# Kernel optimization log

Measured on AMD Instinct MI355X. Metric: run time of the kernel, lower is better.

Reference implementation:

```python
import jax, jax.numpy as jnp
import numpy as np

B_, S_, D_ = 2, 1024, 1024
EXPAND = 2
D_INNER = EXPAND * D_            # 2048
HEADDIM = 64
NHEADS = D_INNER // HEADDIM      # 32
D_STATE = 64
NGROUPS = 1
D_CONV = 4
CONV_DIM = D_INNER + 2 * NGROUPS * D_STATE      # 2176
D_IN_PROJ = 2 * D_INNER + 2 * NGROUPS * D_STATE + NHEADS  # 4256
H_MLP = 8 * D_                   # GatedMLP fc_1 out (scale * d_model)


def setup_inputs() -> dict:
    key = jax.random.key(0)
    ks = jax.random.split(key, 12)
    n = lambda k, shp, s=0.02: jax.random.normal(k, shp, dtype=jnp.float32) * s
    return {
        "x": jax.random.normal(ks[0], (B_, S_, D_), dtype=jnp.float32),
        "in_proj_w": n(ks[1], (D_IN_PROJ, D_)),
        "conv_w": n(ks[2], (CONV_DIM, D_CONV), 0.2),
        "conv_b": jnp.zeros((CONV_DIM,), jnp.float32),
        "dt_bias": jax.random.normal(ks[3], (NHEADS,), dtype=jnp.float32) * 0.5 - 2.0,
        "A_log": jnp.log(1.0 + 15.0 * jax.random.uniform(ks[4], (NHEADS,), dtype=jnp.float32)),
        "D": jax.random.normal(ks[5], (NHEADS,), dtype=jnp.float32) * 0.1 + 1.0,
        "ssm_norm_w": jnp.ones((D_INNER,), jnp.float32),
        "out_proj_w": n(ks[6], (D_, D_INNER)),
        "rms_w": jnp.ones((D_,), jnp.float32),
        "fc1_w": n(ks[7], (H_MLP, D_)),
        "fc2_w": n(ks[8], (D_, H_MLP // 2)),
    }


def _rms(x, w, eps=1e-5):
    return x * jax.lax.rsqrt(jnp.mean(x * x, axis=-1, keepdims=True) + eps) * w


def _mamba(x, in_proj_w, conv_w, conv_b, dt_bias, A_log, D, ssm_norm_w, out_proj_w):
    b, s, _ = x.shape
    zxbcdt = x @ in_proj_w.T                         # [b,s,D_IN_PROJ]
    z = zxbcdt[..., :D_INNER]
    xBC = zxbcdt[..., D_INNER:D_INNER + CONV_DIM]
    dt_raw = zxbcdt[..., -NHEADS:]
    # causal depthwise conv1d + SiLU
    xc = jnp.pad(jnp.transpose(xBC, (0, 2, 1)), ((0, 0), (0, 0), (D_CONV - 1, 0)))
    xc = jax.lax.conv_general_dilated(xc, conv_w[:, None, :], (1,), 'VALID',
                                      feature_group_count=CONV_DIM,
                                      dimension_numbers=('NCH', 'OIH', 'NCH'))
    xBC = jax.nn.silu(jnp.transpose(xc, (0, 2, 1)) + conv_b)
    xs = xBC[..., :D_INNER].reshape(b, s, NHEADS, HEADDIM)
    Bm = xBC[..., D_INNER:D_INNER + D_STATE]         # [b,s,n] (ngroups=1)
    Cm = xBC[..., D_INNER + D_STATE:]
    dt = jax.nn.softplus(dt_raw + dt_bias)           # [b,s,h]
    dA = jnp.exp(dt * (-jnp.exp(A_log)))             # [b,s,h]
    dtx = dt[..., None] * xs                          # [b,s,h,p]

    def step(h, inp):
        dA_t, dtx_t, B_t, C_t = inp
        h = h * dA_t[:, :, None, None] + jnp.einsum('bhp,bn->bhpn', dtx_t, B_t)
        y = jnp.einsum('bhpn,bn->bhp', h, C_t)
        return h, y

    h0 = jnp.zeros((b, NHEADS, HEADDIM, D_STATE), x.dtype)
    _, y = jax.lax.scan(step, h0, (jnp.transpose(dA, (1, 0, 2)),
                                   jnp.transpose(dtx, (1, 0, 2, 3)),
                                   jnp.transpose(Bm, (1, 0, 2)),
                                   jnp.transpose(Cm, (1, 0, 2))))
    y = jnp.transpose(y, (1, 0, 2, 3)) + D[None, None, :, None] * xs
    y = y.reshape(b, s, D_INNER) * jax.nn.silu(z)    # gated
    y = _rms(y, ssm_norm_w)
    return y @ out_proj_w.T


def reference(x, in_proj_w, conv_w, conv_b, dt_bias, A_log, D, ssm_norm_w,
              out_proj_w, rms_w, fc1_w, fc2_w):
    # x = x + mamba(x)
    x = x + _mamba(x, in_proj_w, conv_w, conv_b, dt_bias, A_log, D, ssm_norm_w, out_proj_w)
    # x = x + GatedMLP(RMSNorm(x))
    xn = _rms(x, rms_w)
    h1 = xn @ fc1_w.T
    a, g = jnp.split(h1, 2, axis=-1)
    m = (a * jax.nn.silu(g)) @ fc2_w.T
    return x + m
```

## Files before the change

### kernel.cpp

```cpp
#include <hip/hip_runtime.h>
#include <math.h>

typedef unsigned short u16;
typedef __attribute__((ext_vector_type(8))) __bf16 bf16x8;
typedef __attribute__((ext_vector_type(4))) float f32x4;
typedef __attribute__((ext_vector_type(4))) u16 u16x4;
typedef __attribute__((ext_vector_type(8))) u16 u16x8;
typedef __attribute__((ext_vector_type(4))) float float4v;

constexpr int kS = 1024;
constexpr int kD = 1024;
constexpr int kDinner = 2048;
constexpr int kHeads = 32;
constexpr int kConvDim = 2176;
constexpr int kDproj = 4256;
constexpr int kDprojPad = 4352;
constexpr int kRows = 2048;
constexpr int kHmlp = 8192;
constexpr int kHhalf = 4096;
constexpr int kL = 64;
constexpr int kNC = 16;

__device__ __forceinline__ float bf2f(u16 u) {
    return __builtin_bit_cast(float, (unsigned int)u << 16);
}
__device__ __forceinline__ u16 f2bf(float f) {
    unsigned int u = __builtin_bit_cast(unsigned int, f);
    u += 0x7fffu + ((u >> 16) & 1u);
    return (u16)(u >> 16);
}
__device__ __forceinline__ float silu_(float x) { return x / (1.f + __expf(-x)); }

__device__ __forceinline__ void gld16(const u16* g, u16* l) {
    __builtin_amdgcn_global_load_lds(
        (const __attribute__((address_space(1))) void*)g,
        (__attribute__((address_space(3))) void*)l, 16, 0, 0);
}

constexpr int kB1 = kRows * kD / 4;
constexpr int kB2 = kB1 + kDprojPad * kD / 4;
constexpr int kB3 = kB2 + kD * kDinner / 4;
constexpr int kB4 = kB3 + kHmlp * kD / 4;
constexpr int kB5 = kB4 + kD * kHhalf / 4;
__global__ __launch_bounds__(256)
void cast_all_kernel(const float* __restrict__ x, const float* __restrict__ w1,
                     const float* __restrict__ w2, const float* __restrict__ w3,
                     const float* __restrict__ w4, u16* __restrict__ xbf,
                     u16* __restrict__ w1bf, u16* __restrict__ w2bf,
                     u16* __restrict__ w3bf, u16* __restrict__ w4bf) {
    int i = blockIdx.x * 256 + threadIdx.x;
    const float* src;
    u16* dst;
    int j;
    if (i < kB1) {
        j = i; src = x; dst = xbf;
    } else if (i < kB2) {
        j = i - kB1;
        int e = j * 4, row = e >> 10, col = e & 1023;
        u16x4 o = {0, 0, 0, 0};
        if (row < kDproj) {
            float4v v = *(const float4v*)(w1 + (size_t)row * kD + col);
            o.x = f2bf(v.x); o.y = f2bf(v.y); o.z = f2bf(v.z); o.w = f2bf(v.w);
        }
        ((u16x4*)w1bf)[j] = o;
        return;
    } else if (i < kB3) {
        j = i - kB2; src = w2; dst = w2bf;
    } else if (i < kB4) {
        j = i - kB3;
        int e = j * 4, row = e >> 10, col4 = (e & 1023) >> 2;
        int p = (row < kHhalf) ? row : row - kHhalf;
        int permrow = (p >> 4) * 32 + (p & 15) + ((row < kHhalf) ? 0 : 16);
        float4v v = ((const float4v*)w3)[j];
        u16x4 o;
        o.x = f2bf(v.x); o.y = f2bf(v.y); o.z = f2bf(v.z); o.w = f2bf(v.w);
        ((u16x4*)w3bf)[permrow * 256 + col4] = o;
        return;
    } else {
        j = i - kB4; src = w4; dst = w4bf;
    }
    float4v v = ((const float4v*)src)[j];
    u16x4 o;
    o.x = f2bf(v.x); o.y = f2bf(v.y); o.z = f2bf(v.z); o.w = f2bf(v.w);
    ((u16x4*)dst)[j] = o;
}

template <bool OUT_BF16, bool GATED = false>
__global__ __launch_bounds__(256)
void gemm_bt(const u16* __restrict__ A, const u16* __restrict__ W,
             void* __restrict__ Cout, const float* __restrict__ resid,
             int M, int N, int K) {
    __shared__ u16 As[2][128 * 32];
    __shared__ u16 Bs[2][128 * 32];
    const int tid = threadIdx.x;
    const int lane = tid & 63;
    const int w = __builtin_amdgcn_readfirstlane(tid >> 6);
    const int wm = w >> 1, wn = w & 1;
    const int bm = blockIdx.y * 128;
    const int bn = blockIdx.x * 128;
    const int z = blockIdx.z;
    const int Kchunk = K / gridDim.z;
    const int k0 = z * Kchunk;

    f32x4 acc[4][4];
#pragma unroll
    for (int i = 0; i < 4; i++)
#pragma unroll
        for (int j = 0; j < 4; j++) acc[i][j] = {0.f, 0.f, 0.f, 0.f};

    const int srow = lane >> 2;
    const int scol = (lane & 3) * 8;
    const u16* gA = A + (size_t)(bm + w * 32 + srow) * K + k0 + scol;
    const u16* gB = W + (size_t)(bn + w * 32 + srow) * K + k0 + scol;
    const size_t rstep = (size_t)16 * K;

    const int sbase0 = (w * 32) * 32;
    const int sbase1 = (w * 32 + 16) * 32;
    const int fra = (lane & 15) * 32 + (lane >> 4) * 8;

    gld16(gA, &As[0][sbase0]);
    gld16(gA + rstep, &As[0][sbase1]);
    gld16(gB, &Bs[0][sbase0]);
    gld16(gB + rstep, &Bs[0][sbase1]);

    const int nk = Kchunk >> 5;
    for (int i = 0; i < nk; i++) {
        const int cur = i & 1, nxt = cur ^ 1;
        __syncthreads();
        if (i + 1 < nk) {
            int kt2 = (i + 1) * 32;
            gld16(gA + kt2, &As[nxt][sbase0]);
            gld16(gA + kt2 + rstep, &As[nxt][sbase1]);
            gld16(gB + kt2, &Bs[nxt][sbase0]);
            gld16(gB + kt2 + rstep, &Bs[nxt][sbase1]);
        }
        bf16x8 av[4], bv[4];
#pragma unroll
        for (int mi = 0; mi < 4; mi++)
            av[mi] = *(const bf16x8*)&As[cur][(wm * 64 + mi * 16) * 32 + fra];
#pragma unroll
        for (int ni = 0; ni < 4; ni++)
            bv[ni] = *(const bf16x8*)&Bs[cur][(wn * 64 + ni * 16) * 32 + fra];
#pragma unroll
        for (int mi = 0; mi < 4; mi++)
#pragma unroll
            for (int ni = 0; ni < 4; ni++)
                acc[mi][ni] = __builtin_amdgcn_mfma_f32_16x16x32_bf16(av[mi], bv[ni], acc[mi][ni], 0, 0, 0);
    }

    const int rb = bm + wm * 64 + ((lane >> 4) << 2);
    const int cb = bn + wn * 64 + (lane & 15);
    if (GATED) {
        u16* Cb = (u16*)Cout;
        const int NG = N >> 1;
        const int gc0 = ((bn + wn * 64) >> 1) + (lane & 15);
#pragma unroll
        for (int mi = 0; mi < 4; mi++) {
#pragma unroll
            for (int p = 0; p < 2; p++) {
#pragma unroll
                for (int r = 0; r < 4; r++) {
                    float a = acc[mi][2 * p][r];
                    float g = acc[mi][2 * p + 1][r];
                    Cb[(size_t)(rb + mi * 16 + r) * NG + gc0 + p * 16] =
                        f2bf(a * silu_(g));
                }
            }
        }
        return;
    }
    float* Cf = (float*)Cout + (size_t)z * M * N;
    u16* Cb = (u16*)Cout;
#pragma unroll
    for (int mi = 0; mi < 4; mi++) {
#pragma unroll
        for (int ni = 0; ni < 4; ni++) {
#pragma unroll
            for (int r = 0; r < 4; r++) {
                size_t offo = (size_t)(rb + mi * 16 + r) * N + (cb + ni * 16);
                float v = acc[mi][ni][r];
                if (resid) v += resid[offo];
                if (OUT_BF16) Cb[offo] = f2bf(v);
                else Cf[offo] = v;
            }
        }
    }
}

#define VMCNT10 asm volatile("s_waitcnt vmcnt(10)" ::: "memory")
#define VMCNT0  asm volatile("s_waitcnt vmcnt(0)" ::: "memory")

__global__ __launch_bounds__(512, 2)
void gemm256_gated(const u16* __restrict__ A, const u16* __restrict__ W,
                   u16* __restrict__ Cout, int M, int N, int K) {
    __shared__ u16 lds[2][2][2][2][4096];
    const int tid = threadIdx.x;
    const int lane = tid & 63;
    const int w = __builtin_amdgcn_readfirstlane(tid >> 6);
    const int wm = w >> 2;
    const int wn = w & 3;
    const int wnh = wn >> 1, wnl = wn & 1;

    const int lin = blockIdx.x;
    const int xcd = lin & 7, j = lin >> 3;
    const int bm = (((xcd >> 2) << 2) + (j & 3)) << 8;
    const int bn = (((xcd & 3) << 3) + (j >> 2)) << 8;

    const int rst = tid >> 2, sst = tid & 3;
    const int vst = (((rst >> 1) & 1) << 1) | ((rst >> 2) & 1);
    const u16* gA0 = A + (size_t)(bm + rst) * K + ((sst ^ vst) << 3);
    const u16* gB0 = W + (size_t)(bn + rst) * K + ((sst ^ vst) << 3);
    const size_t hstep = (size_t)128 * K;
    const int wq512 = w * 512;

    const int r0a = lane & 15, slot = lane >> 4;
    const int v2a = (((r0a >> 1) & 1) << 1) | ((r0a >> 2) & 1);
    const int fro = r0a * 32 + ((slot ^ v2a) << 3);

    f32x4 acc[8][4];
#pragma unroll
    for (int i = 0; i < 8; i++)
#pragma unroll
        for (int j_ = 0; j_ < 4; j_++) acc[i][j_] = {0.f, 0.f, 0.f, 0.f};
    bf16x8 bv[4];
    const int nt = K >> 6;

#define STAGE(d, mat, kh, kt)                                               \
    { const u16* g_ = ((mat) ? gB0 : gA0) + (size_t)(kt) * 64 + (kh) * 32;  \
      gld16(g_, &lds[d][mat][0][kh][wq512]);                                \
      gld16(g_ + hstep, &lds[d][mat][1][kh][wq512]); }

#define LDA_FRAG(dst, d, kh, mfb)                                           \
    _Pragma("unroll") for (int i_ = 0; i_ < 4; i_++)                        \
        dst[i_] = *(const bf16x8*)&lds[d][0][wm][kh][((mfb) + i_) * 512 + fro];

#define LDB_FRAG(d, kh)                                                     \
    _Pragma("unroll") for (int i_ = 0; i_ < 4; i_++)                        \
        bv[i_] = *(const bf16x8*)&lds[d][1][wnh][kh][wnl * 2048 + i_ * 512 + fro];

#define PHASE_TAIL(g4, ...)                                                 \
    __builtin_amdgcn_s_barrier();                                           \
    asm volatile("s_waitcnt lgkmcnt(0)" ::: "memory");                      \
    __builtin_amdgcn_s_setprio(1);                                          \
    _Pragma("unroll") for (int i_ = 0; i_ < 4; i_++)                        \
        _Pragma("unroll") for (int n_ = 0; n_ < 4; n_++)                    \
            acc[(g4) * 4 + i_][n_] = __builtin_amdgcn_mfma_f32_16x16x32_bf16( \
                av[i_], bv[n_], acc[(g4) * 4 + i_][n_], 0, 0, 0);           \
    __builtin_amdgcn_s_setprio(0);                                          \
    __VA_ARGS__;                                                            \
    __builtin_amdgcn_s_barrier();

#define TILE(T, D)                                                          \
    {                                             \
      { bf16x8 av[4]; LDB_FRAG(D, 0); LDA_FRAG(av, D, 0, 0);                \
        if ((T) + 1 < nt) STAGE(D ^ 1, 0, 1, (T) + 1);                      \
        PHASE_TAIL(0, ((void)0)) }                                          \
                                             \
      { bf16x8 av[4]; LDA_FRAG(av, D, 0, 4);                                \
        if ((T) + 2 < nt) STAGE(D, 1, 0, (T) + 2);                          \
        PHASE_TAIL(1, if ((T) + 2 < nt) { VMCNT10; } else { VMCNT0; }) }    \
                                                  \
      { bf16x8 av[4]; LDB_FRAG(D, 1); LDA_FRAG(av, D, 1, 0);                \
        if ((T) + 2 < nt) STAGE(D, 0, 0, (T) + 2);                          \
        PHASE_TAIL(0, ((void)0)) }                                          \
                                             \
      { bf16x8 av[4]; LDA_FRAG(av, D, 1, 4);                                \
        if ((T) + 2 < nt) STAGE(D, 1, 1, (T) + 2);                          \
        PHASE_TAIL(1, if ((T) + 2 < nt) { VMCNT10; }                        \
                      else if ((T) + 1 < nt) { VMCNT0; }) }                 \
    }

    STAGE(0, 1, 0, 0);
    STAGE(0, 0, 0, 0);
    STAGE(0, 1, 1, 0);
    STAGE(0, 0, 1, 0);
    STAGE(1, 1, 0, 1);
    STAGE(1, 0, 0, 1);
    STAGE(1, 1, 1, 1);
    VMCNT10;
    __builtin_amdgcn_s_barrier();

    for (int tt = 0; tt < nt; tt += 2) {
        TILE(tt, 0)
        TILE(tt + 1, 1)
    }

#undef TILE
#undef PHASE_TAIL
#undef LDB_FRAG
#undef LDA_FRAG
#undef STAGE

    u16* Cb = Cout;
    const int NG = N >> 1;
    const int rb = bm + wm * 128 + ((lane >> 4) << 2);
    const int gc0 = ((bn + wn * 64) >> 1) + (lane & 15);
#pragma unroll
    for (int mf = 0; mf < 8; mf++) {
#pragma unroll
        for (int p = 0; p < 2; p++) {
#pragma unroll
            for (int r = 0; r < 4; r++) {
                float a = acc[mf][2 * p][r];
                float g = acc[mf][2 * p + 1][r];
                Cb[(size_t)(rb + mf * 16 + r) * NG + gc0 + p * 16] =
                    f2bf(a * silu_(g));
            }
        }
    }
}

__global__ __launch_bounds__(256)
void splitk_reduce_kernel(const float* __restrict__ Cp, const float* __restrict__ resid,
                          float* __restrict__ out, int mn4) {
    int i = blockIdx.x * 256 + threadIdx.x;
    if (i >= mn4) return;
    constexpr size_t MN = (size_t)kRows * kD;
    float4v s0 = ((const float4v*)Cp)[i];
    float4v s1 = ((const float4v*)(Cp + MN))[i];
    float4v s2 = ((const float4v*)(Cp + 2 * MN))[i];
    float4v s3 = ((const float4v*)(Cp + 3 * MN))[i];
    float4v r = ((const float4v*)resid)[i];
    float4v o;
    o.x = s0.x + s1.x + s2.x + s3.x + r.x;
    o.y = s0.y + s1.y + s2.y + s3.y + r.y;
    o.z = s0.z + s1.z + s2.z + s3.z + r.z;
    o.w = s0.w + s1.w + s2.w + s3.w + r.w;
    ((float4v*)out)[i] = o;
}

__global__ __launch_bounds__(256)
void reduce_rms_kernel(const float* __restrict__ Cp, const float* __restrict__ resid,
                       float* __restrict__ x2, const float* __restrict__ rmsw,
                       u16* __restrict__ xnbf) {
    const int row = blockIdx.x;
    const int tid = threadIdx.x;
    constexpr size_t MN = (size_t)kRows * kD;
    size_t i = (size_t)row * (kD / 4) + tid;
    float4v s0 = ((const float4v*)Cp)[i];
    float4v s1 = ((const float4v*)(Cp + MN))[i];
    float4v s2 = ((const float4v*)(Cp + 2 * MN))[i];
    float4v s3 = ((const float4v*)(Cp + 3 * MN))[i];
    float4v r = ((const float4v*)resid)[i];
    float4v v;
    v.x = s0.x + s1.x + s2.x + s3.x + r.x;
    v.y = s0.y + s1.y + s2.y + s3.y + r.y;
    v.z = s0.z + s1.z + s2.z + s3.z + r.z;
    v.w = s0.w + s1.w + s2.w + s3.w + r.w;
    ((float4v*)x2)[i] = v;
    float ss = v.x * v.x + v.y * v.y + v.z * v.z + v.w * v.w;
#pragma unroll
    for (int off = 32; off > 0; off >>= 1) ss += __shfl_down(ss, off);
    __shared__ float red[4];
    int wv = tid >> 6, lane = tid & 63;
    if (lane == 0) red[wv] = ss;
    __syncthreads();
    ss = red[0] + red[1] + red[2] + red[3];
    float rstd = rsqrtf(ss * (1.f / kD) + 1e-5f);
    float4v wv4 = ((const float4v*)rmsw)[tid];
    u16x4 o;
    o.x = f2bf(v.x * rstd * wv4.x);
    o.y = f2bf(v.y * rstd * wv4.y);
    o.z = f2bf(v.z * rstd * wv4.z);
    o.w = f2bf(v.w * rstd * wv4.w);
    ((u16x4*)xnbf)[i] = o;
}

__global__ __launch_bounds__(256)
void convdt_kernel(const u16* __restrict__ zxbf, const float* __restrict__ convw,
                   const float* __restrict__ convb, u16* __restrict__ xsbf,
                   float* __restrict__ BCf, const float* __restrict__ dt_bias,
                   const float* __restrict__ A_log, float* __restrict__ dtf,
                   float* __restrict__ dAf) {
    int c = blockIdx.x * 256 + threadIdx.x;
    int row = blockIdx.y;
    if (c >= kConvDim + kHeads) return;
    if (c < kConvDim) {
        int s = row & (kS - 1);
        float acc = convb[c];
#pragma unroll
        for (int j = 0; j < 4; j++) {
            int sj = s - 3 + j;
            if (sj >= 0)
                acc += bf2f(zxbf[(size_t)(row - 3 + j) * kDprojPad + kDinner + c]) * convw[c * 4 + j];
        }
        float v = silu_(acc);
        if (c < kDinner) xsbf[(size_t)row * kDinner + c] = f2bf(v);
        else BCf[(size_t)row * 128 + (c - kDinner)] = v;
    } else {
        int h = c - kConvDim;
        float raw = bf2f(zxbf[(size_t)row * kDprojPad + (kDinner + kConvDim) + h]) + dt_bias[h];
        float dt = (raw > 20.f) ? raw : log1pf(__expf(raw));
        float dA = __expf(-dt * __expf(A_log[h]));
        dtf[(size_t)row * kHeads + h] = dt;
        dAf[(size_t)row * kHeads + h] = dA;
    }
}

__global__ __launch_bounds__(256)
void scan_chunk_kernel(const u16* __restrict__ xsbf, const float* __restrict__ BCf,
                       const float* __restrict__ dtf, const float* __restrict__ dAf,
                       const float* __restrict__ Dv, u16* __restrict__ ysbf,
                       float* __restrict__ Pf, float* __restrict__ Scf) {
    const int c = blockIdx.x, h = blockIdx.y, b = blockIdx.z;
    const int tid = threadIdx.x;
    const int lane = tid & 63;
    const int nq = tid >> 6;
    const int p = nq * 16 + (lane & 15);
    const int ng = lane >> 4;

    __shared__ float BC_lds[kL * 136];
    __shared__ u16 xs_lds[kL * 64];
    __shared__ float dA_lds[kL];
    __shared__ float dt_lds[kL];
    __shared__ u16 ybuf[kL * 64];

    const int row0 = b * kS + c * kL;

#pragma unroll
    for (int i = 0; i < 8; i++) {
        int e4 = i * 256 + tid;
        int t = e4 >> 5;
        int col = (e4 & 31) * 4;
        float4v v = *(const float4v*)(BCf + (size_t)(row0 + t) * 128 + col);
        int dst = t * 136 + (col < 64 ? col : col + 4);
        *(float4v*)&BC_lds[dst] = v;
    }
#pragma unroll
    for (int i = 0; i < 2; i++) {
        int e8 = i * 256 + tid;
        int t = e8 >> 3, col8 = (e8 & 7) * 8;
        *(u16x8*)&xs_lds[t * 64 + col8] =
            *(const u16x8*)(xsbf + (size_t)(row0 + t) * kDinner + h * 64 + col8);
    }
    if (tid < kL) {
        dt_lds[tid] = dtf[(size_t)(row0 + tid) * kHeads + h];
        dA_lds[tid] = dAf[(size_t)(row0 + tid) * kHeads + h];
    }
    __syncthreads();

    float hst[16];
#pragma unroll
    for (int j = 0; j < 16; j++) hst[j] = 0.f;
    float P = 1.f;
    const float Dh = Dv[h];

    for (int t = 0; t < kL; t++) {
        float dAv = dA_lds[t];
        float dtv = dt_lds[t];
        float xsv = bf2f(xs_lds[t * 64 + p]);
        float dtx = dtv * xsv;
        P *= dAv;
        const float* Bt = &BC_lds[t * 136 + ng * 16];
        const float* Ct = Bt + 68;
        float yp = 0.f;
#pragma unroll
        for (int j = 0; j < 16; j++) {
            float Bn = Bt[j];
            float Cn = Ct[j];
            hst[j] = hst[j] * dAv + dtx * Bn;
            yp += hst[j] * Cn;
        }
        yp += __shfl_xor(yp, 16);
        yp += __shfl_xor(yp, 32);
        if (ng == 0) ybuf[t * 64 + p] = f2bf(yp + Dh * xsv);
        if (tid == 0) Pf[(size_t)(row0 + t) * kHeads + h] = P;
    }
    __syncthreads();

#pragma unroll
    for (int i = 0; i < 2; i++) {
        int e8 = i * 256 + tid;
        int t = e8 >> 3, col8 = (e8 & 7) * 8;
        *(u16x8*)(ysbf + (size_t)(row0 + t) * kDinner + h * 64 + col8) =
            *(u16x8*)&ybuf[t * 64 + col8];
    }
    const int bhc = (b * 32 + h) * kNC + c;
    float* Sdst = Scf + (size_t)bhc * 4096 + p * 64 + ng * 16;
#pragma unroll
    for (int j = 0; j < 16; j += 4) {
        f32x4 v = {hst[j], hst[j + 1], hst[j + 2], hst[j + 3]};
        *(f32x4*)(Sdst + j) = v;
    }
}

__global__ __launch_bounds__(256)
void chunk_state_kernel(const float* __restrict__ Scf, const float* __restrict__ Pf,
                        float* __restrict__ Hinf) {
    const int bh = blockIdx.x;
    const int b = bh >> 5, h = bh & 31;
    const int tid = threadIdx.x;
    float hreg[16];
#pragma unroll
    for (int k = 0; k < 16; k++) hreg[k] = 0.f;
    for (int c = 0; c < kNC - 1; c++) {
        float Q = Pf[(size_t)(b * kS + c * kL + kL - 1) * kHeads + h];
        size_t sbase = (size_t)(bh * kNC + c) * 4096;
        size_t dbase = (size_t)(bh * kNC + c + 1) * 4096;
#pragma unroll
        for (int k = 0; k < 16; k++) {
            float s = Scf[sbase + k * 256 + tid];
            hreg[k] = Q * hreg[k] + s;
            Hinf[dbase + k * 256 + tid] = hreg[k];
        }
    }
}

__global__ __launch_bounds__(256)
void chunk_corr_kernel(const float* __restrict__ Hinf, const float* __restrict__ BCf,
                       const float* __restrict__ Pf, u16* __restrict__ ysbf) {
    const int c = blockIdx.x + 1;
    const int h = blockIdx.y, b = blockIdx.z;
    const int tid = threadIdx.x;
    const int lane = tid & 63, wq = tid >> 6;
    __shared__ float Hin_lds[64 * 65];
    __shared__ float C_lds[kL * 64];
    const int bh = b * 32 + h;
    const size_t hbase = (size_t)(bh * kNC + c) * 4096;
#pragma unroll
    for (int k = 0; k < 16; k++) {
        int e = k * 256 + tid;
        Hin_lds[(e >> 6) * 65 + (e & 63)] = Hinf[hbase + e];
    }
    const int row0 = b * kS + c * kL;
#pragma unroll
    for (int k = 0; k < 4; k++) {
        int e4 = k * 256 + tid;
        int t = e4 >> 4, n4 = (e4 & 15) * 4;
        *(float4v*)&C_lds[t * 64 + n4] =
            *(const float4v*)(BCf + (size_t)(row0 + t) * 128 + 64 + n4);
    }
    __syncthreads();

    float hr[64];
#pragma unroll
    for (int n = 0; n < 64; n++) hr[n] = Hin_lds[lane * 65 + n];

    for (int tt = 0; tt < 16; tt++) {
        int t = wq * 16 + tt;
        float corr = 0.f;
#pragma unroll
        for (int n4 = 0; n4 < 16; n4++) {
            float4v cv = *(const float4v*)&C_lds[t * 64 + n4 * 4];
            corr += cv.x * hr[n4 * 4] + cv.y * hr[n4 * 4 + 1] +
                    cv.z * hr[n4 * 4 + 2] + cv.w * hr[n4 * 4 + 3];
        }
        float Pt = Pf[(size_t)(row0 + t) * kHeads + h];
        size_t yoff = (size_t)(row0 + t) * kDinner + h * 64 + lane;
        ysbf[yoff] = f2bf(bf2f(ysbf[yoff]) + Pt * corr);
    }
}

__global__ __launch_bounds__(256)
void gatenorm_kernel(const u16* __restrict__ ysbf, const u16* __restrict__ zxbf,
                     const float* __restrict__ normw, u16* __restrict__ ybf) {
    const int row = blockIdx.x;
    const int tid = threadIdx.x;
    float v[8];
    float ss = 0.f;
#pragma unroll
    for (int i = 0; i < 8; i++) {
        int idx = i * 256 + tid;
        float y = bf2f(ysbf[(size_t)row * kDinner + idx]);
        float z = bf2f(zxbf[(size_t)row * kDprojPad + idx]);
        v[i] = y * silu_(z);
        ss += v[i] * v[i];
    }
#pragma unroll
    for (int off = 32; off > 0; off >>= 1) ss += __shfl_down(ss, off);
    __shared__ float red[4];
    int wv = tid >> 6, lane = tid & 63;
    if (lane == 0) red[wv] = ss;
    __syncthreads();
    ss = red[0] + red[1] + red[2] + red[3];
    float rstd = rsqrtf(ss * (1.f / kDinner) + 1e-5f);
#pragma unroll
    for (int i = 0; i < 8; i++) {
        int idx = i * 256 + tid;
        ybf[(size_t)row * kDinner + idx] = f2bf(v[i] * rstd * normw[idx]);
    }
}

extern "C" void kernel_launch(void* const* d_in, const int* in_sizes, int n_in,
                              void* d_out, int out_size, void* d_ws, size_t ws_size,
                              hipStream_t stream) {
    const float* x         = (const float*)d_in[0];
    const float* in_proj_w = (const float*)d_in[1];
    const float* conv_w    = (const float*)d_in[2];
    const float* conv_b    = (const float*)d_in[3];
    const float* dt_bias   = (const float*)d_in[4];
    const float* A_log     = (const float*)d_in[5];
    const float* Dvec      = (const float*)d_in[6];
    const float* ssm_norm_w= (const float*)d_in[7];
    const float* out_proj_w= (const float*)d_in[8];
    const float* rms_w     = (const float*)d_in[9];
    const float* fc1_w     = (const float*)d_in[10];
    const float* fc2_w     = (const float*)d_in[11];
    float* out = (float*)d_out;

    char* ws = (char*)d_ws;
    size_t off = 0;
    auto alloc = [&](size_t bytes) -> void* {
        void* p = ws + off;
        off += (bytes + 255) & ~(size_t)255;
        return p;
    };
    u16*   xbf  = (u16*)alloc((size_t)kRows * kD * 2);
    u16*   w1bf = (u16*)alloc((size_t)kDprojPad * kD * 2);
    u16*   w2bf = (u16*)alloc((size_t)kD * kDinner * 2);
    u16*   w3bf = (u16*)alloc((size_t)kHmlp * kD * 2);
    u16*   w4bf = (u16*)alloc((size_t)kD * kHhalf * 2);
    u16*   zxbf = (u16*)alloc((size_t)kRows * kDprojPad * 2);
    u16*   xsbf = (u16*)alloc((size_t)kRows * kDinner * 2);
    float* BCf  = (float*)alloc((size_t)kRows * 128 * 4);
    float* dtf  = (float*)alloc((size_t)kRows * kHeads * 4);
    float* dAf  = (float*)alloc((size_t)kRows * kHeads * 4);
    float* Pf   = (float*)alloc((size_t)kRows * kHeads * 4);
    u16*   ysbf = (u16*)alloc((size_t)kRows * kDinner * 2);
    u16*   ybf  = (u16*)alloc((size_t)kRows * kDinner * 2);
    float* x2   = (float*)alloc((size_t)kRows * kD * 4);
    u16*   xnbf = (u16*)alloc((size_t)kRows * kD * 2);
    u16*   h1bf = (u16*)alloc((size_t)kRows * kHmlp * 2);
    u16*   gbf  = (u16*)alloc((size_t)kRows * kHhalf * 2);
    float* Scf  = (float*)gbf;
    float* Hinf = (float*)h1bf;
    float* Cp   = (float*)h1bf;
    (void)ws_size; (void)in_sizes; (void)n_in; (void)out_size;

    cast_all_kernel<<<kB5 / 256, 256, 0, stream>>>(
        x, in_proj_w, out_proj_w, fc1_w, fc2_w, xbf, w1bf, w2bf, w3bf, w4bf);

    gemm_bt<true><<<dim3(kDprojPad / 128, kRows / 128, 1), 256, 0, stream>>>(
        xbf, w1bf, zxbf, nullptr, kRows, kDprojPad, kD);

    convdt_kernel<<<dim3((kConvDim + kHeads + 255) / 256, kRows), 256, 0, stream>>>(
        zxbf, conv_w, conv_b, xsbf, BCf, dt_bias, A_log, dtf, dAf);

    scan_chunk_kernel<<<dim3(kNC, kHeads, 2), 256, 0, stream>>>(
        xsbf, BCf, dtf, dAf, Dvec, ysbf, Pf, Scf);
    chunk_state_kernel<<<64, 256, 0, stream>>>(Scf, Pf, Hinf);
    chunk_corr_kernel<<<dim3(kNC - 1, kHeads, 2), 256, 0, stream>>>(Hinf, BCf, Pf, ysbf);

    gatenorm_kernel<<<kRows, 256, 0, stream>>>(ysbf, zxbf, ssm_norm_w, ybf);

    gemm_bt<false><<<dim3(kD / 128, kRows / 128, 4), 256, 0, stream>>>(
        ybf, w2bf, Cp, nullptr, kRows, kD, kDinner);
    reduce_rms_kernel<<<kRows, 256, 0, stream>>>(Cp, x, x2, rms_w, xnbf);

    gemm256_gated<<<dim3((kRows >> 8) * (kHmlp >> 8)), 512, 0, stream>>>(
        xnbf, w3bf, gbf, kRows, kHmlp, kD);

    gemm_bt<false><<<dim3(kD / 128, kRows / 128, 4), 256, 0, stream>>>(
        gbf, w4bf, Cp, nullptr, kRows, kD, kHhalf);
    splitk_reduce_kernel<<<(kRows * kD / 4 + 255) / 256, 256, 0, stream>>>(
        Cp, x2, out, kRows * kD / 4);
}
```

Baseline: 366.2 us.

## Replace sequential intra-chunk scan with SSD-style MFMA matmuls using split-bf16 precision

The per-chunk selective scan used to loop over 64 timesteps serially. It is rewritten as the chunked SSD formulation: a causal C·Bᵀ Gram matrix with decay masking, then M·X for the outputs and a weighted Xᵀ·B for the chunk-end state, all on bf16 MFMA. Hi/lo bf16 splitting keeps near-fp32 accuracy. The decay is now computed in-kernel from a prefix sum of dt, so the dA buffer and its write from the conv kernel are dropped. This adds about 64KB of LDS per block, which can limit occupancy, plus extra MFMA passes for the precision split.

```diff
diff --git a/kernel.cpp b/kernel.cpp
--- a/kernel.cpp
+++ b/kernel.cpp
@@ -370,8 +370,7 @@
 void convdt_kernel(const u16* __restrict__ zxbf, const float* __restrict__ convw,
                    const float* __restrict__ convb, u16* __restrict__ xsbf,
                    float* __restrict__ BCf, const float* __restrict__ dt_bias,
-                   const float* __restrict__ A_log, float* __restrict__ dtf,
-                   float* __restrict__ dAf) {
+                   float* __restrict__ dtf) {
     int c = blockIdx.x * 256 + threadIdx.x;
     int row = blockIdx.y;
     if (c >= kConvDim + kHeads) return;
@@ -391,96 +390,193 @@
         int h = c - kConvDim;
         float raw = bf2f(zxbf[(size_t)row * kDprojPad + (kDinner + kConvDim) + h]) + dt_bias[h];
         float dt = (raw > 20.f) ? raw : log1pf(__expf(raw));
-        float dA = __expf(-dt * __expf(A_log[h]));
         dtf[(size_t)row * kHeads + h] = dt;
-        dAf[(size_t)row * kHeads + h] = dA;
     }
 }
 
 __global__ __launch_bounds__(256)
 void scan_chunk_kernel(const u16* __restrict__ xsbf, const float* __restrict__ BCf,
-                       const float* __restrict__ dtf, const float* __restrict__ dAf,
+                       const float* __restrict__ dtf, const float* __restrict__ A_log,
                        const float* __restrict__ Dv, u16* __restrict__ ysbf,
                        float* __restrict__ Pf, float* __restrict__ Scf) {
+    constexpr int LDT = 72;
+    __shared__ __align__(16) char smem[65280];
+    u16* Chi  = (u16*)(smem);
+    u16* Clo  = (u16*)(smem + 9216);
+    u16* Bhi  = (u16*)(smem + 18432);
+    u16* Blo  = (u16*)(smem + 27648);
+    u16* BThi = (u16*)(smem + 36864);
+    u16* BTlo = (u16*)(smem + 46080);
+    u16* xT   = (u16*)(smem + 55296);
+    float* laS  = (float*)(smem + 64512);
+    float* dtS  = (float*)(smem + 64768);
+    float* wscS = (float*)(smem + 65024);
+    u16* Mhi  = Clo;
+    u16* Mlo  = Bhi;
+    u16* ybuf = Chi;
+
     const int c = blockIdx.x, h = blockIdx.y, b = blockIdx.z;
     const int tid = threadIdx.x;
     const int lane = tid & 63;
-    const int nq = tid >> 6;
-    const int p = nq * 16 + (lane & 15);
-    const int ng = lane >> 4;
-
-    __shared__ float BC_lds[kL * 136];
-    __shared__ u16 xs_lds[kL * 64];
-    __shared__ float dA_lds[kL];
-    __shared__ float dt_lds[kL];
-    __shared__ u16 ybuf[kL * 64];
-
+    const int w = __builtin_amdgcn_readfirstlane(tid >> 6);
     const int row0 = b * kS + c * kL;
-
-#pragma unroll
-    for (int i = 0; i < 8; i++) {
-        int e4 = i * 256 + tid;
-        int t = e4 >> 5;
-        int col = (e4 & 31) * 4;
+    const int frow = lane & 15;
+    const int fk = (lane >> 4) * 8;
+    const int q4 = (lane >> 4) * 4;
+    const int w16 = w * 16;
+
+#pragma unroll
+    for (int k = 0; k < 8; k++) {
+        int e4 = k * 256 + tid;
+        int t = e4 >> 5, col = (e4 & 31) * 4;
         float4v v = *(const float4v*)(BCf + (size_t)(row0 + t) * 128 + col);
-        int dst = t * 136 + (col < 64 ? col : col + 4);
-        *(float4v*)&BC_lds[dst] = v;
-    }
-#pragma unroll
-    for (int i = 0; i < 2; i++) {
-        int e8 = i * 256 + tid;
-        int t = e8 >> 3, col8 = (e8 & 7) * 8;
-        *(u16x8*)&xs_lds[t * 64 + col8] =
-            *(const u16x8*)(xsbf + (size_t)(row0 + t) * kDinner + h * 64 + col8);
-    }
-    if (tid < kL) {
-        dt_lds[tid] = dtf[(size_t)(row0 + tid) * kHeads + h];
-        dA_lds[tid] = dAf[(size_t)(row0 + tid) * kHeads + h];
+        u16x4 hi, lo;
+        hi.x = f2bf(v.x); lo.x = f2bf(v.x - bf2f(hi.x));
+        hi.y = f2bf(v.y); lo.y = f2bf(v.y - bf2f(hi.y));
+        hi.z = f2bf(v.z); lo.z = f2bf(v.z - bf2f(hi.z));
+        hi.w = f2bf(v.w); lo.w = f2bf(v.w - bf2f(hi.w));
+        int cc = col & 63;
+        u16* dh = (col < 64) ? Bhi : Chi;
+        u16* dl = (col < 64) ? Blo : Clo;
+        *(u16x4*)&dh[t * LDT + cc] = hi;
+        *(u16x4*)&dl[t * LDT + cc] = lo;
+    }
+#pragma unroll
+    for (int k = 0; k < 2; k++) {
+        int e8 = k * 256 + tid;
+        int t = e8 >> 3, p8 = (e8 & 7) * 8;
+        u16x8 xv = *(const u16x8*)(xsbf + (size_t)(row0 + t) * kDinner + h * 64 + p8);
+#pragma unroll
+        for (int j = 0; j < 8; j++) xT[(p8 + j) * LDT + t] = xv[j];
+    }
+    if (tid < 64) {
+        float d = dtf[(size_t)(row0 + tid) * kHeads + h];
+        dtS[tid] = d;
+        float cs = d;
+#pragma unroll
+        for (int off = 1; off < 64; off <<= 1) {
+            float o = __shfl_up(cs, off);
+            if (lane >= off) cs += o;
+        }
+        float A_h = __expf(A_log[h]);
+        float la = -A_h * cs;
+        laS[tid] = la;
+        Pf[(size_t)(row0 + tid) * kHeads + h] = __expf(la);
+        float la63 = __shfl(la, 63);
+        wscS[tid] = d * __expf(la63 - la);
     }
     __syncthreads();
 
-    float hst[16];
-#pragma unroll
-    for (int j = 0; j < 16; j++) hst[j] = 0.f;
-    float P = 1.f;
+    f32x4 accG[4];
+#pragma unroll
+    for (int i = 0; i < 4; i++) accG[i] = {0.f, 0.f, 0.f, 0.f};
+#pragma unroll
+    for (int kb = 0; kb < 2; kb++) {
+        bf16x8 ch = *(const bf16x8*)&Chi[(w16 + frow) * LDT + kb * 32 + fk];
+        bf16x8 cl = *(const bf16x8*)&Clo[(w16 + frow) * LDT + kb * 32 + fk];
+#pragma unroll
+        for (int nt = 0; nt < 4; nt++) {
+            if (nt <= w) {
+                bf16x8 bh = *(const bf16x8*)&Bhi[(nt * 16 + frow) * LDT + kb * 32 + fk];
+                bf16x8 bl = *(const bf16x8*)&Blo[(nt * 16 + frow) * LDT + kb * 32 + fk];
+                accG[nt] = __builtin_amdgcn_mfma_f32_16x16x32_bf16(ch, bh, accG[nt], 0, 0, 0);
+                accG[nt] = __builtin_amdgcn_mfma_f32_16x16x32_bf16(ch, bl, accG[nt], 0, 0, 0);
+                accG[nt] = __builtin_amdgcn_mfma_f32_16x16x32_bf16(cl, bh, accG[nt], 0, 0, 0);
+            }
+        }
+    }
+#pragma unroll
+    for (int k = 0; k < 16; k++) {
+        int e = k * 256 + tid;
+        int s = e >> 6, n = e & 63;
+        BThi[n * LDT + s] = Bhi[s * LDT + n];
+        BTlo[n * LDT + s] = Blo[s * LDT + n];
+    }
+    __syncthreads();
+
+    f32x4 la4 = *(const f32x4*)&laS[w16 + q4];
+#pragma unroll
+    for (int nt = 0; nt < 4; nt++) {
+        int s = nt * 16 + frow;
+        float las = laS[s], dts = dtS[s];
+#pragma unroll
+        for (int r = 0; r < 4; r++) {
+            int t = w16 + q4 + r;
+            float f = 0.f;
+            if (nt <= w && s <= t)
+                f = dts * __expf(la4[r] - las) * accG[nt][r];
+            u16 mh = f2bf(f);
+            u16 ml = f2bf(f - bf2f(mh));
+            Mhi[t * LDT + s] = mh;
+            Mlo[t * LDT + s] = ml;
+        }
+    }
+
+    f32x4 accY[4];
+#pragma unroll
+    for (int i = 0; i < 4; i++) accY[i] = {0.f, 0.f, 0.f, 0.f};
+#pragma unroll
+    for (int kb = 0; kb < 2; kb++) {
+        bf16x8 mh = *(const bf16x8*)&Mhi[(w16 + frow) * LDT + kb * 32 + fk];
+        bf16x8 ml = *(const bf16x8*)&Mlo[(w16 + frow) * LDT + kb * 32 + fk];
+#pragma unroll
+        for (int nt = 0; nt < 4; nt++) {
+            bf16x8 xv = *(const bf16x8*)&xT[(nt * 16 + frow) * LDT + kb * 32 + fk];
+            accY[nt] = __builtin_amdgcn_mfma_f32_16x16x32_bf16(mh, xv, accY[nt], 0, 0, 0);
+            accY[nt] = __builtin_amdgcn_mfma_f32_16x16x32_bf16(ml, xv, accY[nt], 0, 0, 0);
+        }
+    }
+
+    f32x4 accS[4];
+#pragma unroll
+    for (int i = 0; i < 4; i++) accS[i] = {0.f, 0.f, 0.f, 0.f};
+#pragma unroll
+    for (int kb = 0; kb < 2; kb++) {
+        u16x8 xu = __builtin_bit_cast(u16x8, *(const bf16x8*)&xT[(w16 + frow) * LDT + kb * 32 + fk]);
+        f32x4 w0v = *(const f32x4*)&wscS[kb * 32 + fk];
+        f32x4 w1v = *(const f32x4*)&wscS[kb * 32 + fk + 4];
+        u16x8 xh, xl;
+#pragma unroll
+        for (int j = 0; j < 8; j++) {
+            float wv = (j < 4) ? w0v[j] : w1v[j - 4];
+            float f = bf2f(xu[j]) * wv;
+            u16 hh = f2bf(f);
+            xh[j] = hh;
+            xl[j] = f2bf(f - bf2f(hh));
+        }
+        bf16x8 xwh = __builtin_bit_cast(bf16x8, xh);
+        bf16x8 xwl = __builtin_bit_cast(bf16x8, xl);
+#pragma unroll
+        for (int nt = 0; nt < 4; nt++) {
+            bf16x8 bh = *(const bf16x8*)&BThi[(nt * 16 + frow) * LDT + kb * 32 + fk];
+            bf16x8 bl = *(const bf16x8*)&BTlo[(nt * 16 + frow) * LDT + kb * 32 + fk];
+            accS[nt] = __builtin_amdgcn_mfma_f32_16x16x32_bf16(xwh, bh, accS[nt], 0, 0, 0);
+            accS[nt] = __builtin_amdgcn_mfma_f32_16x16x32_bf16(xwh, bl, accS[nt], 0, 0, 0);
+            accS[nt] = __builtin_amdgcn_mfma_f32_16x16x32_bf16(xwl, bh, accS[nt], 0, 0, 0);
+        }
+    }
+
     const float Dh = Dv[h];
-
-    for (int t = 0; t < kL; t++) {
-        float dAv = dA_lds[t];
-        float dtv = dt_lds[t];
-        float xsv = bf2f(xs_lds[t * 64 + p]);
-        float dtx = dtv * xsv;
-        P *= dAv;
-        const float* Bt = &BC_lds[t * 136 + ng * 16];
-        const float* Ct = Bt + 68;
-        float yp = 0.f;
-#pragma unroll
-        for (int j = 0; j < 16; j++) {
-            float Bn = Bt[j];
-            float Cn = Ct[j];
-            hst[j] = hst[j] * dAv + dtx * Bn;
-            yp += hst[j] * Cn;
-        }
-        yp += __shfl_xor(yp, 16);
-        yp += __shfl_xor(yp, 32);
-        if (ng == 0) ybuf[t * 64 + p] = f2bf(yp + Dh * xsv);
-        if (tid == 0) Pf[(size_t)(row0 + t) * kHeads + h] = P;
+    const int bhc = (b * 32 + h) * kNC + c;
+    float* Sb = Scf + (size_t)bhc * 4096;
+#pragma unroll
+    for (int nt = 0; nt < 4; nt++) {
+#pragma unroll
+        for (int r = 0; r < 4; r++) {
+            int t = w16 + q4 + r;
+            int pc = nt * 16 + frow;
+            float y = accY[nt][r] + Dh * bf2f(xT[pc * LDT + t]);
+            ybuf[t * 64 + pc] = f2bf(y);
+            Sb[t * 64 + pc] = accS[nt][r];
+        }
     }
     __syncthreads();
-
-#pragma unroll
-    for (int i = 0; i < 2; i++) {
-        int e8 = i * 256 + tid;
+#pragma unroll
+    for (int k = 0; k < 2; k++) {
+        int e8 = k * 256 + tid;
         int t = e8 >> 3, col8 = (e8 & 7) * 8;
         *(u16x8*)(ysbf + (size_t)(row0 + t) * kDinner + h * 64 + col8) =
             *(u16x8*)&ybuf[t * 64 + col8];
-    }
-    const int bhc = (b * 32 + h) * kNC + c;
-    float* Sdst = Scf + (size_t)bhc * 4096 + p * 64 + ng * 16;
-#pragma unroll
-    for (int j = 0; j < 16; j += 4) {
-        f32x4 v = {hst[j], hst[j + 1], hst[j + 2], hst[j + 3]};
-        *(f32x4*)(Sdst + j) = v;
     }
 }
 
@@ -614,7 +710,6 @@
     u16*   xsbf = (u16*)alloc((size_t)kRows * kDinner * 2);
     float* BCf  = (float*)alloc((size_t)kRows * 128 * 4);
     float* dtf  = (float*)alloc((size_t)kRows * kHeads * 4);
-    float* dAf  = (float*)alloc((size_t)kRows * kHeads * 4);
     float* Pf   = (float*)alloc((size_t)kRows * kHeads * 4);
     u16*   ysbf = (u16*)alloc((size_t)kRows * kDinner * 2);
     u16*   ybf  = (u16*)alloc((size_t)kRows * kDinner * 2);
@@ -634,10 +729,10 @@
         xbf, w1bf, zxbf, nullptr, kRows, kDprojPad, kD);
 
     convdt_kernel<<<dim3((kConvDim + kHeads + 255) / 256, kRows), 256, 0, stream>>>(
-        zxbf, conv_w, conv_b, xsbf, BCf, dt_bias, A_log, dtf, dAf);
+        zxbf, conv_w, conv_b, xsbf, BCf, dt_bias, dtf);
 
     scan_chunk_kernel<<<dim3(kNC, kHeads, 2), 256, 0, stream>>>(
-        xsbf, BCf, dtf, dAf, Dvec, ysbf, Pf, Scf);
+        xsbf, BCf, dtf, A_log, Dvec, ysbf, Pf, Scf);
     chunk_state_kernel<<<64, 256, 0, stream>>>(Scf, Pf, Hinf);
     chunk_corr_kernel<<<dim3(kNC - 1, kHeads, 2), 256, 0, stream>>>(Hinf, BCf, Pf, ysbf);
 
```

After: 344.0 us. -6.1%, faster.
